# Optimization experiments

Hardware: AMD Instinct MI355X
Metric: run time of the kernel (lower is better)

The kernel has to match this reference:

```python
import jax, jax.numpy as jnp
import numpy as np

DIM = 768
NUM_HEADS = 12
HEAD_DIM = DIM // NUM_HEADS
SCALE = HEAD_DIM ** (-0.5)


def setup_inputs() -> dict:
    key = jax.random.key(0)
    ks = jax.random.split(key, 8)
    B, Nq, Nk, Nv = 2, 2048, 2048, 2048
    init = 0.02
    return {
        "xq": jax.random.normal(ks[0], (B, Nq, DIM), dtype=jnp.float32),
        "xk": jax.random.normal(ks[1], (B, Nk, DIM), dtype=jnp.float32),
        "xv": jax.random.normal(ks[2], (B, Nv, DIM), dtype=jnp.float32),
        # torch nn.Linear weights are [out_features, in_features]; qkv_bias=False
        "Wq": jax.random.normal(ks[3], (DIM, DIM), dtype=jnp.float32) * init,
        "Wk": jax.random.normal(ks[4], (DIM, DIM), dtype=jnp.float32) * init,
        "Wv": jax.random.normal(ks[5], (DIM, DIM), dtype=jnp.float32) * init,
        "Wp": jax.random.normal(ks[6], (DIM, DIM), dtype=jnp.float32) * init,
        "bp": jax.random.normal(ks[7], (DIM,), dtype=jnp.float32) * init,
    }


def reference(xq, xk, xv, Wq, Wk, Wv, Wp, bp):
    B, Nq, C = xq.shape
    H, D = NUM_HEADS, HEAD_DIM
    # linear projections (torch Linear: x @ W.T), split heads -> [B, H, N, D]
    q = (xq @ Wq.T).reshape(B, Nq, H, D).transpose(0, 2, 1, 3)
    k = (xk @ Wk.T).reshape(B, xk.shape[1], H, D).transpose(0, 2, 1, 3)
    v = (xv @ Wv.T).reshape(B, xv.shape[1], H, D).transpose(0, 2, 1, 3)
    # attention scores [B, H, Nq, Nk]
    attn = jnp.einsum("bhqd,bhkd->bhqk", q, k) * SCALE
    attn = jax.nn.softmax(attn, axis=-1)
    # weighted values -> merge heads [B, Nq, C]
    out = jnp.einsum("bhqk,bhkd->bhqd", attn, v)
    out = out.transpose(0, 2, 1, 3).reshape(B, Nq, C)
    return out @ Wp.T + bp
```

## Files before the change

### kernel.cpp

```cpp
#include <hip/hip_runtime.h>
#include <hip/hip_bf16.h>


#define NSEQ 2048
#define CDIM 768
#define NH   12
#define HD   64
#define MTOT 4096
#define XEL  (MTOT*CDIM)
#define WEL  (CDIM*CDIM)
#define X8   (XEL/8)
#define W8   (WEL/8)
#define PSTR 72
#define QSCALE 0.18033688011112042f

typedef __attribute__((ext_vector_type(8))) short bf16x8;
typedef __attribute__((ext_vector_type(4))) float floatx4;

static __device__ __forceinline__ unsigned short f2bf(float f) {
  union { float f; unsigned int u; } v; v.f = f;
  return (unsigned short)((v.u + 0x8000u) >> 16);
}
static __device__ __forceinline__ unsigned pk2bf(float a, float b) {
  unsigned ua = __float_as_uint(a) + 0x8000u;
  unsigned ub = __float_as_uint(b) + 0x8000u;
  return __builtin_amdgcn_perm(ub, ua, 0x07060302);
}

static __device__ __forceinline__ void lds16(const void* g, void* l) {
  __builtin_amdgcn_global_load_lds(
      (const __attribute__((address_space(1))) unsigned int*)g,
      (__attribute__((address_space(3))) unsigned int*)l, 16, 0, 0);
}

__global__ __launch_bounds__(256) void cast_all(
    const float* __restrict__ xq, const float* __restrict__ xk,
    const float* __restrict__ xv, const float* __restrict__ wq,
    const float* __restrict__ wk, const float* __restrict__ wv,
    const float* __restrict__ wp,
    unsigned short* __restrict__ Xq, unsigned short* __restrict__ Xk,
    unsigned short* __restrict__ Xv, unsigned short* __restrict__ Wq,
    unsigned short* __restrict__ Wk, unsigned short* __restrict__ Wv,
    unsigned short* __restrict__ Wp) {
  int i = blockIdx.x * 256 + threadIdx.x;
  const float* s; unsigned short* d; int off;
  if (i < 3 * X8) {
    int t = i / X8; off = i - t * X8;
    s = (t == 0) ? xq : (t == 1) ? xk : xv;
    d = (t == 0) ? Xq : (t == 1) ? Xk : Xv;
  } else {
    int j = i - 3 * X8; int t = j / W8; off = j - t * W8;
    s = (t == 0) ? wq : (t == 1) ? wk : (t == 2) ? wv : wp;
    d = (t == 0) ? Wq : (t == 1) ? Wk : (t == 2) ? Wv : Wp;
  }
  const float4* sp = (const float4*)s + (size_t)off * 2;
  float4 a = sp[0], b = sp[1];
  uint4 o;
  o.x = pk2bf(a.x, a.y); o.y = pk2bf(a.z, a.w);
  o.z = pk2bf(b.x, b.y); o.w = pk2bf(b.z, b.w);
  *(uint4*)(d + (size_t)off * 8) = o;
}

__global__ __launch_bounds__(256) void gemm_qkv(
    const unsigned short* __restrict__ Xq, const unsigned short* __restrict__ Xk,
    const unsigned short* __restrict__ Xv, const unsigned short* __restrict__ Wq,
    const unsigned short* __restrict__ Wk, const unsigned short* __restrict__ Wv,
    unsigned short* __restrict__ Qo, unsigned short* __restrict__ Ko,
    unsigned short* __restrict__ Vo) {
  int z = blockIdx.z;
  const unsigned short* A; const unsigned short* B; int m0, n0;
  if (z == 0)      { A = Xq; B = Wq; m0 = blockIdx.y * 128; n0 = blockIdx.x * 128; }
  else if (z == 1) { A = Xk; B = Wk; m0 = blockIdx.y * 128; n0 = blockIdx.x * 128; }
  else             { A = Wv; B = Xv; m0 = blockIdx.x * 128; n0 = blockIdx.y * 128; }
  __shared__ __align__(16) unsigned short As[128 * 64];
  __shared__ __align__(16) unsigned short Bs[128 * 64];
  int tid = threadIdx.x, lane = tid & 63, wave = tid >> 6;
  int quad = lane >> 4, l15 = lane & 15, l7 = l15 & 7;
  int wm = (wave >> 1) * 64, wn = (wave & 1) * 64;
  floatx4 acc[4][4];
#pragma unroll
  for (int i = 0; i < 4; i++)
#pragma unroll
    for (int j = 0; j < 4; j++) acc[i][j] = (floatx4){0.f, 0.f, 0.f, 0.f};

  for (int k0 = 0; k0 < CDIM; k0 += 64) {
#pragma unroll
    for (int i = 0; i < 4; i++) {
      int idx = i * 256 + tid;
      int R = idx >> 3, c = (idx & 7) ^ (R & 7);
      lds16(A + (size_t)(m0 + R) * CDIM + k0 + c * 8, &As[idx * 8]);
      lds16(B + (size_t)(n0 + R) * CDIM + k0 + c * 8, &Bs[idx * 8]);
    }
    __syncthreads();
#pragma unroll
    for (int ks = 0; ks < 2; ks++) {
      int csw = ((ks * 4 + quad) ^ l7) * 8;
      bf16x8 af[4], bfr[4];
#pragma unroll
      for (int i = 0; i < 4; i++)
        af[i] = *(const bf16x8*)&As[(wm + i * 16 + l15) * 64 + csw];
#pragma unroll
      for (int i = 0; i < 4; i++)
        bfr[i] = *(const bf16x8*)&Bs[(wn + i * 16 + l15) * 64 + csw];
#pragma unroll
      for (int mi = 0; mi < 4; mi++)
#pragma unroll
        for (int ni = 0; ni < 4; ni++)
          acc[mi][ni] = __builtin_amdgcn_mfma_f32_16x16x32_bf16(
              af[mi], bfr[ni], acc[mi][ni], 0, 0, 0);
    }
    __syncthreads();
  }
#pragma unroll
  for (int mi = 0; mi < 4; mi++) {
#pragma unroll
    for (int ni = 0; ni < 4; ni++) {
#pragma unroll
      for (int r = 0; r < 4; r++) {
        int grow = m0 + wm + mi * 16 + quad * 4 + r;
        int gcol = n0 + wn + ni * 16 + l15;
        float v = acc[mi][ni][r];
        if (z == 0) {
          int b = grow >> 11, nq = grow & 2047, h = gcol >> 6, d = gcol & 63;
          Qo[((size_t)(b * NH + h) * NSEQ + nq) * HD + d] = f2bf(v * QSCALE);
        } else if (z == 1) {
          int b = grow >> 11, nq = grow & 2047, h = gcol >> 6, d = gcol & 63;
          Ko[((size_t)(b * NH + h) * NSEQ + nq) * HD + d] = f2bf(v);
        } else {
          int b = gcol >> 11, nq = gcol & 2047;
          Vo[((size_t)b * CDIM + grow) * NSEQ + nq] = f2bf(v);
        }
      }
    }
  }
}

__global__ __launch_bounds__(256, 3) void attn_kernel(
    const unsigned short* __restrict__ Q, const unsigned short* __restrict__ K,
    const unsigned short* __restrict__ Vt, unsigned short* __restrict__ ctx) {
  int qt = blockIdx.x, bh = blockIdx.y;
  int tid = threadIdx.x, lane = tid & 63, wave = tid >> 6;
  int half = wave >> 1, qsub = wave & 1;
  int quad = lane >> 4, l15 = lane & 15, l7 = l15 & 7;
  __shared__ __align__(16) unsigned short Ks[2][64 * 64];
  __shared__ __align__(16) unsigned short Vs[2][64 * 64];
  __shared__ __align__(16) unsigned short Ps[4][16 * PSTR];

  const unsigned short* Qg = Q + ((size_t)bh * NSEQ + qt * 64 + qsub * 32) * HD;
  const unsigned short* Kg = K + ((size_t)bh * NSEQ + half * 1024) * HD;
  const unsigned short* Vg = Vt + (size_t)bh * HD * NSEQ + half * 1024;

  bf16x8 qf[2][2];
#pragma unroll
  for (int qi = 0; qi < 2; qi++)
#pragma unroll
    for (int ks = 0; ks < 2; ks++)
      qf[qi][ks] = *(const bf16x8*)(Qg + (qi * 16 + l15) * HD + ks * 32 + quad * 8);

  int tid2 = tid & 127;
  int kgo[4], vgo[4], ldst[4];
#pragma unroll
  for (int i = 0; i < 4; i++) {
    int idx = i * 128 + tid2;
    int R = idx >> 3, c = (idx & 7) ^ (R & 7);
    kgo[i] = R * HD + c * 8;
    vgo[i] = R * NSEQ + c * 8;
    ldst[i] = idx * 8;
  }
  unsigned short* Ksh = Ks[half];
  unsigned short* Vsh = Vs[half];
  unsigned short* Pw = &Ps[wave][0];

  float lacc[2] = {0.f, 0.f};
  floatx4 o[2][4];
#pragma unroll
  for (int qi = 0; qi < 2; qi++)
#pragma unroll
    for (int dt = 0; dt < 4; dt++) o[qi][dt] = (floatx4){0.f, 0.f, 0.f, 0.f};

  for (int t = 0; t < 16; t++) {
    int k0 = t * 64;
#pragma unroll
    for (int i = 0; i < 4; i++) {
      lds16(Kg + (size_t)k0 * HD + kgo[i], &Ksh[ldst[i]]);
      lds16(Vg + k0 + vgo[i], &Vsh[ldst[i]]);
    }
    __syncthreads();
    bf16x8 kf[4][2], vf[4][2];
#pragma unroll
    for (int nt = 0; nt < 4; nt++)
#pragma unroll
      for (int x = 0; x < 2; x++)
        kf[nt][x] = *(const bf16x8*)&Ksh[(nt * 16 + l15) * 64 + ((x * 4 + quad) ^ l7) * 8];
#pragma unroll
    for (int dt = 0; dt < 4; dt++)
#pragma unroll
      for (int x = 0; x < 2; x++)
        vf[dt][x] = *(const bf16x8*)&Vs[half][(dt * 16 + l15) * 64 + ((x * 4 + quad) ^ l7) * 8];
#pragma unroll
    for (int qi = 0; qi < 2; qi++) {
#pragma unroll
      for (int nt = 0; nt < 4; nt++) {
        floatx4 st = (floatx4){0.f, 0.f, 0.f, 0.f};
        st = __builtin_amdgcn_mfma_f32_16x16x32_bf16(kf[nt][0], qf[qi][0], st, 0, 0, 0);
        st = __builtin_amdgcn_mfma_f32_16x16x32_bf16(kf[nt][1], qf[qi][1], st, 0, 0, 0);
        float p0 = __builtin_exp2f(st[0]), p1 = __builtin_exp2f(st[1]);
        float p2 = __builtin_exp2f(st[2]), p3 = __builtin_exp2f(st[3]);
        lacc[qi] += (p0 + p1) + (p2 + p3);
        *(uint2*)&Pw[l15 * PSTR + nt * 16 + quad * 4] =
            make_uint2(pk2bf(p0, p1), pk2bf(p2, p3));
      }
#pragma unroll
      for (int ks = 0; ks < 2; ks++) {
        bf16x8 pf = *(const bf16x8*)&Pw[l15 * PSTR + ks * 32 + quad * 8];
#pragma unroll
        for (int dt = 0; dt < 4; dt++)
          o[qi][dt] = __builtin_amdgcn_mfma_f32_16x16x32_bf16(vf[dt][ks], pf, o[qi][dt], 0, 0, 0);
      }
    }
    __syncthreads();
  }
#pragma unroll
  for (int qi = 0; qi < 2; qi++) {
    lacc[qi] += __shfl_xor(lacc[qi], 16, 64);
    lacc[qi] += __shfl_xor(lacc[qi], 32, 64);
  }
  float* Obuf = (float*)&Ks[0][0];
  float* Lbuf = (float*)&Ps[0][0];
  if (half == 1) {
#pragma unroll
    for (int qi = 0; qi < 2; qi++) {
      int ro = qsub * 32 + qi * 16 + l15;
#pragma unroll
      for (int dt = 0; dt < 4; dt++)
        *(floatx4*)&Obuf[ro * 64 + dt * 16 + quad * 4] = o[qi][dt];
      if (quad == 0) Lbuf[ro] = lacc[qi];
    }
  }
  __syncthreads();
  if (half == 0) {
    int b = bh / NH, h = bh - b * NH;
#pragma unroll
    for (int qi = 0; qi < 2; qi++) {
      int ro = qsub * 32 + qi * 16 + l15;
      float inv = 1.f / (lacc[qi] + Lbuf[ro]);
      int qrow = qt * 64 + ro;
      size_t gbase = (size_t)(b * NSEQ + qrow) * CDIM + h * HD + quad * 4;
#pragma unroll
      for (int dt = 0; dt < 4; dt++) {
        floatx4 ob = *(floatx4*)&Obuf[ro * 64 + dt * 16 + quad * 4];
        float v0 = (o[qi][dt][0] + ob[0]) * inv, v1 = (o[qi][dt][1] + ob[1]) * inv;
        float v2 = (o[qi][dt][2] + ob[2]) * inv, v3 = (o[qi][dt][3] + ob[3]) * inv;
        *(uint2*)&ctx[gbase + dt * 16] = make_uint2(pk2bf(v0, v1), pk2bf(v2, v3));
      }
    }
  }
}

__global__ __launch_bounds__(256) void gemm_out(
    const unsigned short* __restrict__ A, const unsigned short* __restrict__ B,
    const float* __restrict__ bias, float* __restrict__ out) {
  int m0 = blockIdx.y * 64, n0 = blockIdx.x * 64;
  __shared__ __align__(16) unsigned short As[64 * 128];
  __shared__ __align__(16) unsigned short Bs[64 * 128];
  int tid = threadIdx.x, lane = tid & 63, wave = tid >> 6;
  int quad = lane >> 4, l15 = lane & 15, l7 = l15 & 7;
  int wm = (wave >> 1) * 32, wn = (wave & 1) * 32;
  floatx4 acc[2][2];
#pragma unroll
  for (int i = 0; i < 2; i++)
#pragma unroll
    for (int j = 0; j < 2; j++) acc[i][j] = (floatx4){0.f, 0.f, 0.f, 0.f};

  for (int k0 = 0; k0 < CDIM; k0 += 128) {
#pragma unroll
    for (int i = 0; i < 4; i++) {
      int idx = i * 256 + tid;
      int R = idx >> 4, c4 = idx & 15;
      int cs = (c4 & 8) | ((c4 & 7) ^ (R & 7));
      lds16(A + (size_t)(m0 + R) * CDIM + k0 + cs * 8, &As[idx * 8]);
      lds16(B + (size_t)(n0 + R) * CDIM + k0 + cs * 8, &Bs[idx * 8]);
    }
    __syncthreads();
#pragma unroll
    for (int ks = 0; ks < 4; ks++) {
      int c = ks * 4 + quad;
      int csw = ((c & 8) | ((c & 7) ^ l7)) * 8;
      bf16x8 af[2], bfr[2];
#pragma unroll
      for (int i = 0; i < 2; i++)
        af[i] = *(const bf16x8*)&As[(wm + i * 16 + l15) * 128 + csw];
#pragma unroll
      for (int i = 0; i < 2; i++)
        bfr[i] = *(const bf16x8*)&Bs[(wn + i * 16 + l15) * 128 + csw];
#pragma unroll
      for (int mi = 0; mi < 2; mi++)
#pragma unroll
        for (int ni = 0; ni < 2; ni++)
          acc[mi][ni] = __builtin_amdgcn_mfma_f32_16x16x32_bf16(
              af[mi], bfr[ni], acc[mi][ni], 0, 0, 0);
    }
    __syncthreads();
  }
  float bv[2];
#pragma unroll
  for (int ni = 0; ni < 2; ni++) bv[ni] = bias[n0 + wn + ni * 16 + l15];
#pragma unroll
  for (int mi = 0; mi < 2; mi++)
#pragma unroll
    for (int ni = 0; ni < 2; ni++)
#pragma unroll
      for (int r = 0; r < 4; r++) {
        int grow = m0 + wm + mi * 16 + quad * 4 + r;
        int gcol = n0 + wn + ni * 16 + l15;
        out[(size_t)grow * CDIM + gcol] = acc[mi][ni][r] + bv[ni];
      }
}

extern "C" void kernel_launch(void* const* d_in, const int* in_sizes, int n_in,
                              void* d_out, int out_size, void* d_ws, size_t ws_size,
                              hipStream_t stream) {
  const float* xq = (const float*)d_in[0];
  const float* xk = (const float*)d_in[1];
  const float* xv = (const float*)d_in[2];
  const float* wq = (const float*)d_in[3];
  const float* wk = (const float*)d_in[4];
  const float* wv = (const float*)d_in[5];
  const float* wp = (const float*)d_in[6];
  const float* bp = (const float*)d_in[7];
  float* out = (float*)d_out;

  char* p = (char*)d_ws;
  unsigned short* Xq = (unsigned short*)p; p += (size_t)XEL * 2;
  unsigned short* Xk = (unsigned short*)p; p += (size_t)XEL * 2;
  unsigned short* Xv = (unsigned short*)p; p += (size_t)XEL * 2;
  unsigned short* Wq = (unsigned short*)p; p += (size_t)WEL * 2;
  unsigned short* Wk = (unsigned short*)p; p += (size_t)WEL * 2;
  unsigned short* Wv = (unsigned short*)p; p += (size_t)WEL * 2;
  unsigned short* Wp = (unsigned short*)p; p += (size_t)WEL * 2;
  unsigned short* Qb = (unsigned short*)p; p += (size_t)XEL * 2;
  unsigned short* Kb = (unsigned short*)p; p += (size_t)XEL * 2;
  unsigned short* Vb = (unsigned short*)p; p += (size_t)XEL * 2;
  unsigned short* Cx = (unsigned short*)p; p += (size_t)XEL * 2;

  cast_all<<<(3 * X8 + 4 * W8) / 256, 256, 0, stream>>>(
      xq, xk, xv, wq, wk, wv, wp, Xq, Xk, Xv, Wq, Wk, Wv, Wp);

  gemm_qkv<<<dim3(CDIM / 128, MTOT / 128, 3), 256, 0, stream>>>(
      Xq, Xk, Xv, Wq, Wk, Wv, Qb, Kb, Vb);

  attn_kernel<<<dim3(NSEQ / 64, 2 * NH), 256, 0, stream>>>(Qb, Kb, Vb, Cx);

  gemm_out<<<dim3(CDIM / 64, MTOT / 64), 256, 0, stream>>>(Cx, Wp, bp, out);
}
```

Before: 201.4 us.

## Retile QKV GEMM to 128x96 blocks and compute softmax row sums via MFMA

The QKV projection GEMM moves from 128x128 tiles to 128x96 tiles held in one unified shared buffer. This gives 8x32x3 blocks instead of 6x32x3, so more blocks are available to fill the GPU's compute units, at the cost of a smaller per-block tile and less data reuse. In the attention kernel, the per-lane scalar accumulation of softmax denominators and the cross-lane shuffle reduction are replaced by an extra MFMA against a vector of bf16 ones. That takes VALU adds off the exp path, but the row sums are now built from the bf16-rounded probabilities.

```diff
diff --git a/kernel.cpp b/kernel.cpp
--- a/kernel.cpp
+++ b/kernel.cpp
@@ -68,70 +68,102 @@
     unsigned short* __restrict__ Qo, unsigned short* __restrict__ Ko,
     unsigned short* __restrict__ Vo) {
   int z = blockIdx.z;
-  const unsigned short* A; const unsigned short* B; int m0, n0;
-  if (z == 0)      { A = Xq; B = Wq; m0 = blockIdx.y * 128; n0 = blockIdx.x * 128; }
-  else if (z == 1) { A = Xk; B = Wk; m0 = blockIdx.y * 128; n0 = blockIdx.x * 128; }
-  else             { A = Wv; B = Xv; m0 = blockIdx.x * 128; n0 = blockIdx.y * 128; }
-  __shared__ __align__(16) unsigned short As[128 * 64];
-  __shared__ __align__(16) unsigned short Bs[128 * 64];
+  const unsigned short* A; const unsigned short* B; int am0, bn0, RA;
+  if (z == 0)      { A = Xq; B = Wq; am0 = blockIdx.y * 128; bn0 = blockIdx.x * 96; RA = 128; }
+  else if (z == 1) { A = Xk; B = Wk; am0 = blockIdx.y * 128; bn0 = blockIdx.x * 96; RA = 128; }
+  else             { A = Wv; B = Xv; am0 = blockIdx.x * 96;  bn0 = blockIdx.y * 128; RA = 96; }
+  __shared__ __align__(16) unsigned short S[224 * 64];
   int tid = threadIdx.x, lane = tid & 63, wave = tid >> 6;
   int quad = lane >> 4, l15 = lane & 15, l7 = l15 & 7;
-  int wm = (wave >> 1) * 64, wn = (wave & 1) * 64;
-  floatx4 acc[4][4];
-#pragma unroll
-  for (int i = 0; i < 4; i++)
-#pragma unroll
-    for (int j = 0; j < 4; j++) acc[i][j] = (floatx4){0.f, 0.f, 0.f, 0.f};
+
+  const unsigned short* gptr[7]; int ldo[7];
+#pragma unroll
+  for (int i = 0; i < 7; i++) {
+    int idx = i * 256 + tid;
+    int row = idx >> 3, c = (idx & 7) ^ (row & 7);
+    gptr[i] = (row < RA ? A + (size_t)(am0 + row) * CDIM
+                        : B + (size_t)(bn0 + row - RA) * CDIM) + c * 8;
+    ldo[i] = idx * 8;
+  }
+  floatx4 acc[12];
+#pragma unroll
+  for (int i = 0; i < 12; i++) acc[i] = (floatx4){0.f, 0.f, 0.f, 0.f};
 
   for (int k0 = 0; k0 < CDIM; k0 += 64) {
 #pragma unroll
-    for (int i = 0; i < 4; i++) {
-      int idx = i * 256 + tid;
-      int R = idx >> 3, c = (idx & 7) ^ (R & 7);
-      lds16(A + (size_t)(m0 + R) * CDIM + k0 + c * 8, &As[idx * 8]);
-      lds16(B + (size_t)(n0 + R) * CDIM + k0 + c * 8, &Bs[idx * 8]);
-    }
-    __syncthreads();
-#pragma unroll
-    for (int ks = 0; ks < 2; ks++) {
-      int csw = ((ks * 4 + quad) ^ l7) * 8;
-      bf16x8 af[4], bfr[4];
-#pragma unroll
-      for (int i = 0; i < 4; i++)
-        af[i] = *(const bf16x8*)&As[(wm + i * 16 + l15) * 64 + csw];
-#pragma unroll
-      for (int i = 0; i < 4; i++)
-        bfr[i] = *(const bf16x8*)&Bs[(wn + i * 16 + l15) * 64 + csw];
-#pragma unroll
-      for (int mi = 0; mi < 4; mi++)
-#pragma unroll
-        for (int ni = 0; ni < 4; ni++)
-          acc[mi][ni] = __builtin_amdgcn_mfma_f32_16x16x32_bf16(
-              af[mi], bfr[ni], acc[mi][ni], 0, 0, 0);
-    }
-    __syncthreads();
-  }
-#pragma unroll
-  for (int mi = 0; mi < 4; mi++) {
-#pragma unroll
-    for (int ni = 0; ni < 4; ni++) {
-#pragma unroll
-      for (int r = 0; r < 4; r++) {
-        int grow = m0 + wm + mi * 16 + quad * 4 + r;
-        int gcol = n0 + wn + ni * 16 + l15;
-        float v = acc[mi][ni][r];
-        if (z == 0) {
-          int b = grow >> 11, nq = grow & 2047, h = gcol >> 6, d = gcol & 63;
-          Qo[((size_t)(b * NH + h) * NSEQ + nq) * HD + d] = f2bf(v * QSCALE);
-        } else if (z == 1) {
-          int b = grow >> 11, nq = grow & 2047, h = gcol >> 6, d = gcol & 63;
-          Ko[((size_t)(b * NH + h) * NSEQ + nq) * HD + d] = f2bf(v);
-        } else {
-          int b = gcol >> 11, nq = gcol & 2047;
-          Vo[((size_t)b * CDIM + grow) * NSEQ + nq] = f2bf(v);
+    for (int i = 0; i < 7; i++) lds16(gptr[i] + k0, &S[ldo[i]]);
+    __syncthreads();
+    if (z < 2) {
+      int wm = (wave >> 1) * 64, wn = (wave & 1) * 48;
+#pragma unroll
+      for (int ks = 0; ks < 2; ks++) {
+        int csw = ((ks * 4 + quad) ^ l7) * 8;
+        bf16x8 af[4], bfr[3];
+#pragma unroll
+        for (int i = 0; i < 4; i++)
+          af[i] = *(const bf16x8*)&S[(wm + i * 16 + l15) * 64 + csw];
+#pragma unroll
+        for (int j = 0; j < 3; j++)
+          bfr[j] = *(const bf16x8*)&S[(128 + wn + j * 16 + l15) * 64 + csw];
+#pragma unroll
+        for (int mi = 0; mi < 4; mi++)
+#pragma unroll
+          for (int ni = 0; ni < 3; ni++)
+            acc[mi * 3 + ni] = __builtin_amdgcn_mfma_f32_16x16x32_bf16(
+                af[mi], bfr[ni], acc[mi * 3 + ni], 0, 0, 0);
+      }
+    } else {
+      int wm = (wave & 1) * 48, wn = (wave >> 1) * 64;
+#pragma unroll
+      for (int ks = 0; ks < 2; ks++) {
+        int csw = ((ks * 4 + quad) ^ l7) * 8;
+        bf16x8 af[3], bfr[4];
+#pragma unroll
+        for (int i = 0; i < 3; i++)
+          af[i] = *(const bf16x8*)&S[(wm + i * 16 + l15) * 64 + csw];
+#pragma unroll
+        for (int j = 0; j < 4; j++)
+          bfr[j] = *(const bf16x8*)&S[(96 + wn + j * 16 + l15) * 64 + csw];
+#pragma unroll
+        for (int mi = 0; mi < 3; mi++)
+#pragma unroll
+          for (int ni = 0; ni < 4; ni++)
+            acc[mi * 4 + ni] = __builtin_amdgcn_mfma_f32_16x16x32_bf16(
+                af[mi], bfr[ni], acc[mi * 4 + ni], 0, 0, 0);
+      }
+    }
+    __syncthreads();
+  }
+  if (z < 2) {
+    int wm = (wave >> 1) * 64, wn = (wave & 1) * 48;
+#pragma unroll
+    for (int mi = 0; mi < 4; mi++)
+#pragma unroll
+      for (int ni = 0; ni < 3; ni++)
+#pragma unroll
+        for (int r = 0; r < 4; r++) {
+          int grow = am0 + wm + mi * 16 + quad * 4 + r;
+          int gcol = bn0 + wn + ni * 16 + l15;
+          float v = acc[mi * 3 + ni][r];
+          int b = grow >> 11, nq = grow & 2047, h = gcol >> 6, dd = gcol & 63;
+          if (z == 0)
+            Qo[((size_t)(b * NH + h) * NSEQ + nq) * HD + dd] = f2bf(v * QSCALE);
+          else
+            Ko[((size_t)(b * NH + h) * NSEQ + nq) * HD + dd] = f2bf(v);
         }
-      }
-    }
+  } else {
+    int wm = (wave & 1) * 48, wn = (wave >> 1) * 64;
+#pragma unroll
+    for (int mi = 0; mi < 3; mi++)
+#pragma unroll
+      for (int ni = 0; ni < 4; ni++)
+#pragma unroll
+        for (int r = 0; r < 4; r++) {
+          int o = am0 + wm + mi * 16 + quad * 4 + r;
+          int mg = bn0 + wn + ni * 16 + l15;
+          int b = mg >> 11, nq = mg & 2047;
+          Vo[((size_t)b * CDIM + o) * NSEQ + nq] = f2bf(acc[mi * 4 + ni][r]);
+        }
   }
 }
 
@@ -157,6 +189,10 @@
     for (int ks = 0; ks < 2; ks++)
       qf[qi][ks] = *(const bf16x8*)(Qg + (qi * 16 + l15) * HD + ks * 32 + quad * 8);
 
+  bf16x8 ones;
+#pragma unroll
+  for (int i = 0; i < 8; i++) ones[i] = (short)0x3F80;
+
   int tid2 = tid & 127;
   int kgo[4], vgo[4], ldst[4];
 #pragma unroll
@@ -171,12 +207,14 @@
   unsigned short* Vsh = Vs[half];
   unsigned short* Pw = &Ps[wave][0];
 
-  float lacc[2] = {0.f, 0.f};
+  floatx4 ol[2];
   floatx4 o[2][4];
 #pragma unroll
-  for (int qi = 0; qi < 2; qi++)
+  for (int qi = 0; qi < 2; qi++) {
+    ol[qi] = (floatx4){0.f, 0.f, 0.f, 0.f};
 #pragma unroll
     for (int dt = 0; dt < 4; dt++) o[qi][dt] = (floatx4){0.f, 0.f, 0.f, 0.f};
+  }
 
   for (int t = 0; t < 16; t++) {
     int k0 = t * 64;
@@ -196,7 +234,7 @@
     for (int dt = 0; dt < 4; dt++)
 #pragma unroll
       for (int x = 0; x < 2; x++)
-        vf[dt][x] = *(const bf16x8*)&Vs[half][(dt * 16 + l15) * 64 + ((x * 4 + quad) ^ l7) * 8];
+        vf[dt][x] = *(const bf16x8*)&Vsh[(dt * 16 + l15) * 64 + ((x * 4 + quad) ^ l7) * 8];
 #pragma unroll
     for (int qi = 0; qi < 2; qi++) {
 #pragma unroll
@@ -206,24 +244,19 @@
         st = __builtin_amdgcn_mfma_f32_16x16x32_bf16(kf[nt][1], qf[qi][1], st, 0, 0, 0);
         float p0 = __builtin_exp2f(st[0]), p1 = __builtin_exp2f(st[1]);
         float p2 = __builtin_exp2f(st[2]), p3 = __builtin_exp2f(st[3]);
-        lacc[qi] += (p0 + p1) + (p2 + p3);
         *(uint2*)&Pw[l15 * PSTR + nt * 16 + quad * 4] =
             make_uint2(pk2bf(p0, p1), pk2bf(p2, p3));
       }
 #pragma unroll
       for (int ks = 0; ks < 2; ks++) {
         bf16x8 pf = *(const bf16x8*)&Pw[l15 * PSTR + ks * 32 + quad * 8];
+        ol[qi] = __builtin_amdgcn_mfma_f32_16x16x32_bf16(ones, pf, ol[qi], 0, 0, 0);
 #pragma unroll
         for (int dt = 0; dt < 4; dt++)
           o[qi][dt] = __builtin_amdgcn_mfma_f32_16x16x32_bf16(vf[dt][ks], pf, o[qi][dt], 0, 0, 0);
       }
     }
     __syncthreads();
-  }
-#pragma unroll
-  for (int qi = 0; qi < 2; qi++) {
-    lacc[qi] += __shfl_xor(lacc[qi], 16, 64);
-    lacc[qi] += __shfl_xor(lacc[qi], 32, 64);
   }
   float* Obuf = (float*)&Ks[0][0];
   float* Lbuf = (float*)&Ps[0][0];
@@ -234,7 +267,7 @@
 #pragma unroll
       for (int dt = 0; dt < 4; dt++)
         *(floatx4*)&Obuf[ro * 64 + dt * 16 + quad * 4] = o[qi][dt];
-      if (quad == 0) Lbuf[ro] = lacc[qi];
+      if (quad == 0) Lbuf[ro] = ol[qi][0];
     }
   }
   __syncthreads();
@@ -243,7 +276,7 @@
 #pragma unroll
     for (int qi = 0; qi < 2; qi++) {
       int ro = qsub * 32 + qi * 16 + l15;
-      float inv = 1.f / (lacc[qi] + Lbuf[ro]);
+      float inv = 1.f / (ol[qi][0] + Lbuf[ro]);
       int qrow = qt * 64 + ro;
       size_t gbase = (size_t)(b * NSEQ + qrow) * CDIM + h * HD + quad * 4;
 #pragma unroll
@@ -346,7 +379,7 @@
   cast_all<<<(3 * X8 + 4 * W8) / 256, 256, 0, stream>>>(
       xq, xk, xv, wq, wk, wv, wp, Xq, Xk, Xv, Wq, Wk, Wv, Wp);
 
-  gemm_qkv<<<dim3(CDIM / 128, MTOT / 128, 3), 256, 0, stream>>>(
+  gemm_qkv<<<dim3(8, 32, 3), 256, 0, stream>>>(
       Xq, Xk, Xv, Wq, Wk, Wv, Qb, Kb, Vb);
 
   attn_kernel<<<dim3(NSEQ / 64, 2 * NH), 256, 0, stream>>>(Qb, Kb, Vb, Cx);
```

After: 192.2 us. 1.05x faster.
